# Optimization experiments

Measured on AMD Instinct MI355X. Metric: run time of the kernel, lower is better.

The kernel has to match this reference:

```python
import jax, jax.numpy as jnp
import numpy as np

B, N, M, C, H = 2, 256, 512, 256, 8
Dh = C // H          # head dim = 32
F = 256              # frequency_embedding_size
MAX_PERIOD = 10000.0


def setup_inputs() -> dict:
    rng = jax.random.key(0)
    ks = jax.random.split(rng, 12)
    s = 0.02

    def w(k, shape):
        return jax.random.normal(k, shape, jnp.float32) * s

    inp = {
        "query": jax.random.normal(ks[0], (B, N, C), jnp.float32),
        "key": jax.random.normal(ks[1], (B, M, C), jnp.float32),
        "query_pos": jax.random.uniform(ks[2], (B, N, M), jnp.float32),
        # attention projections (torch Linear stores W as (out,in))
        "Wq": w(ks[3], (C, C)), "bq": jnp.zeros((C,), jnp.float32),
        "Wk": w(ks[4], (C, C)),
        "Wv": w(ks[5], (C, C)), "bv": jnp.zeros((C,), jnp.float32),
        "Wo": w(ks[6], (C, C)), "bo": jnp.zeros((C,), jnp.float32),
        # ScalarEmbedder MLP: Linear(F, C) -> SiLU -> Linear(C, C)
        "W1": w(ks[7], (C, F)), "b1": jnp.zeros((C,), jnp.float32),
        "W2": w(ks[8], (C, C)), "b2": jnp.zeros((C,), jnp.float32),
        "freqs": jnp.exp(-np.log(MAX_PERIOD) * jnp.arange(F // 2, dtype=jnp.float32) / (F // 2)),
    }
    return inp


def reference(query, key, query_pos, Wq, bq, Wk, Wv, bv, Wo, bo, W1, b1, W2, b2, freqs):
    scale = Dh ** (-0.5)
    # projections -> (B, H, N/M, Dh)
    q = (query @ Wq.T + bq).reshape(B, N, H, Dh).transpose(0, 2, 1, 3)
    k = (key @ Wk.T).reshape(B, M, H, Dh).transpose(0, 2, 1, 3)
    v = (key @ Wv.T + bv).reshape(B, M, H, Dh).transpose(0, 2, 1, 3)
    # scalar positional embedding per (n, m) pair
    t = query_pos.reshape(-1)                              # (B*N*M,)
    tf = t[:, None] * freqs                                # (B*N*M, F/2)
    emb = jnp.concatenate([jnp.cos(tf), jnp.sin(tf)], -1)  # (B*N*M, F)
    pe = jax.nn.silu(emb @ W1.T + b1) @ W2.T + b2          # (B*N*M, C)
    pe = pe.reshape(B, N, M, H, Dh).transpose(0, 3, 1, 2, 4)  # (B,H,N,M,Dh)
    # gated scores: (q[:,:,:,None] * pe) . k  ==  einsum over d
    attn = jnp.einsum('bhnd,bhnmd,bhmd->bhnm', q, pe, k) * scale
    attn = jax.nn.softmax(attn, axis=-1)
    x = jnp.einsum('bhnm,bhmd->bhnd', attn, v)             # (B,H,N,Dh)
    x = x.transpose(0, 2, 1, 3).reshape(B, N, C)
    return x @ Wo.T + bo + query
```

## Files before the change

### kernel.cpp

```cpp
#include <hip/hip_runtime.h>

#define Bn 2
#define Nn 256
#define Mn 512
#define Cn 256
#define Hn 8
#define MT 128
#define SCALE_ 0.17677669529663687f
#define INV2PI 0.15915494309189535f

typedef short bf16x8 __attribute__((ext_vector_type(8)));
typedef short bf16x4 __attribute__((ext_vector_type(4)));
typedef float f32x4 __attribute__((ext_vector_type(4)));

static __device__ __forceinline__ float b2f(short s) {
    unsigned u = ((unsigned)(unsigned short)s) << 16;
    return __builtin_bit_cast(float, u);
}
static __device__ __forceinline__ short f2b(float f) {
    unsigned u = __builtin_bit_cast(unsigned, f);
    u += 0x7fffu + ((u >> 16) & 1u);
    return (short)(u >> 16);
}
static __device__ __forceinline__ void async16(const void* g, void* l) {
    __builtin_amdgcn_global_load_lds(
        (const __attribute__((address_space(1))) unsigned int*)g,
        (__attribute__((address_space(3))) unsigned int*)l, 16, 0, 0);
}

__global__ __launch_bounds__(256) void prep2(
        const float* __restrict__ key, const float* __restrict__ Wk,
        const float* __restrict__ Wv, const float* __restrict__ bv,
        const float* __restrict__ W1, const float* __restrict__ W2,
        short* __restrict__ W1b, short* __restrict__ W2b,
        short* __restrict__ kpb, short* __restrict__ vpb) {
    __shared__ float arow[32][Cn];
    const int bid = blockIdx.x;
    const int t = threadIdx.x;
    if (bid < 64) {
        const int half = bid >> 5;
        const int off = (bid & 31) * 2048 + t * 8;
        const float* src = half ? W2 : W1;
        short* dst = half ? W2b : W1b;
        const float4 a = *(const float4*)(src + off);
        const float4 c = *(const float4*)(src + off + 4);
        bf16x8 p;
        p[0] = f2b(a.x); p[1] = f2b(a.y); p[2] = f2b(a.z); p[3] = f2b(a.w);
        p[4] = f2b(c.x); p[5] = f2b(c.y); p[6] = f2b(c.z); p[7] = f2b(c.w);
        *(bf16x8*)(dst + off) = p;
        return;
    }
    const int isv = bid >= 320;
    const int id = bid - (isv ? 320 : 64);
    const int r0 = (id >> 3) * 32, c0 = (id & 7) * 32;
    const float* W = isv ? Wv : Wk;
    #pragma unroll
    for (int i = 0; i < 32; ++i) arow[i][t] = key[(size_t)(r0 + i) * Cn + t];
    __syncthreads();
    const int col = c0 + (t & 31);
    const int rs = t >> 5;
    float a4[4] = {0.f, 0.f, 0.f, 0.f};
    const float* wr = W + (size_t)col * Cn;
    for (int k = 0; k < Cn; k += 4) {
        const float4 wv = *(const float4*)(wr + k);
        #pragma unroll
        for (int i = 0; i < 4; ++i) {
            const int r = rs * 4 + i;
            a4[i] += arow[r][k] * wv.x + arow[r][k+1] * wv.y
                   + arow[r][k+2] * wv.z + arow[r][k+3] * wv.w;
        }
    }
    if (!isv) {
        const int bk = r0 >> 9, mm0 = (r0 & 511) + rs * 4;
        char* base = (char*)kpb + (size_t)bk * Mn * Cn * 2;
        #pragma unroll
        for (int i = 0; i < 4; ++i) {
            const int m = mm0 + i;
            *(short*)(base + m * 512 + ((col * 2) ^ ((m & 7) << 4))) = f2b(a4[i]);
        }
    } else {
        const float bvv = bv[col];
        #pragma unroll
        for (int i = 0; i < 4; ++i)
            vpb[(size_t)(r0 + rs * 4 + i) * Cn + col] = f2b(a4[i] + bvv);
    }
}

__global__ __launch_bounds__(512, 1) void fused_attn(
        const float* __restrict__ query, const float* __restrict__ Wq,
        const float* __restrict__ bq, const short* __restrict__ kpb,
        const short* __restrict__ vpb, const float* __restrict__ qpos,
        const short* __restrict__ W1b, const short* __restrict__ W2b,
        const float* __restrict__ b1, const float* __restrict__ b2,
        const float* __restrict__ freqs, const float* __restrict__ Wo,
        const float* __restrict__ bo, float* __restrict__ xout) {
    __shared__ __align__(16) char embS[MT * 512];
    __shared__ __align__(16) char kS[MT * 512];
    __shared__ float tposS[Mn];
    __shared__ float fbuf[128];
    __shared__ float qbuf[Cn];
    __shared__ float b2buf[Cn];
    __shared__ float scb2[Hn * MT];
    __shared__ float pacc[512];
    __shared__ float corrS[Hn], lS[Hn];

    const int t = threadIdx.x;
    const int lane = t & 63;
    const int w = t >> 6;
    const int lr = lane & 15, lg = lane >> 4;

    const int qrow = ((blockIdx.x & 7) << 6) | (blockIdx.x >> 3);
    const int b = qrow >> 8;

    const int cA = w * 32 + lr, cB = cA + 16;
    const short* w1p0 = W1b + (size_t)cA * Cn + lg * 8;
    const short* w1p1 = W1b + (size_t)cB * Cn + lg * 8;
    const short* w2p0 = W2b + (size_t)cA * Cn + lg * 8;
    const short* w2p1 = W2b + (size_t)cB * Cn + lg * 8;
    const float b1v0 = b1[cA], b1v1 = b1[cB];

    tposS[t] = qpos[(size_t)qrow * Mn + t];
    if (t < 128) fbuf[t] = freqs[t] * INV2PI;
    if (t < 256) {
        b2buf[t] = b2[t];
        scb2[t] = query[(size_t)qrow * Cn + t];
    }
    __syncthreads();
    {
        const int c = t & 255, half = t >> 8;
        const float* wr = Wq + (size_t)c * Cn + half * 128;
        const float* xb = scb2 + half * 128;
        float s = 0.f;
        for (int k = 0; k < 128; k += 4) {
            const float4 wv = *(const float4*)(wr + k);
            s += xb[k] * wv.x + xb[k+1] * wv.y + xb[k+2] * wv.z + xb[k+3] * wv.w;
        }
        pacc[t] = s;
    }
    __syncthreads();
    if (t < 256) qbuf[t] = (pacc[t] + pacc[t + 256] + bq[t]) * SCALE_;

    float m_run = -1e30f, l_run = 0.f;
    float xacc = 0.f;
    bf16x8 wreg[16];

    for (int m0 = 0; m0 < Mn; m0 += MT) {
        {
            const size_t tbase = ((size_t)(b * Mn + m0)) * Cn * 2;
            #pragma unroll
            for (int i = 0; i < 8; ++i) {
                const int seg = (i * 8 + w) * 1024;
                async16((const char*)kpb + tbase + seg + lane * 16, kS + seg);
            }
        }

        {
            const int m = t >> 2, fq = t & 3;
            const float tv = tposS[m0 + m];
            char* rowp = embS + m * 512;
            const int sw = (m & 7) << 4;
            #pragma unroll
            for (int j8 = 0; j8 < 4; ++j8) {
                bf16x8 pc, ps;
                #pragma unroll
                for (int e = 0; e < 8; ++e) {
                    const float xr = tv * fbuf[fq * 32 + j8 * 8 + e];
                    pc[e] = f2b(__builtin_amdgcn_cosf(xr));
                    ps[e] = f2b(__builtin_amdgcn_sinf(xr));
                }
                *(bf16x8*)(rowp + ((fq * 64 + j8 * 16) ^ sw)) = pc;
                *(bf16x8*)(rowp + ((256 + fq * 64 + j8 * 16) ^ sw)) = ps;
            }
        }
        __syncthreads();

        {
            int woff = 0;
            asm volatile("" : "+v"(woff));
            #pragma unroll
            for (int kk = 0; kk < 8; ++kk) {
                wreg[kk] = *(const bf16x8*)(w1p0 + woff + kk * 32);
                wreg[8 + kk] = *(const bf16x8*)(w1p1 + woff + kk * 32);
            }
        }
        f32x4 acc[8][2];
        #pragma unroll
        for (int pb = 0; pb < 8; ++pb) {
            acc[pb][0] = (f32x4){0.f, 0.f, 0.f, 0.f};
            acc[pb][1] = (f32x4){0.f, 0.f, 0.f, 0.f};
        }
        #pragma unroll
        for (int pb = 0; pb < 8; ++pb) {
            const int row = pb * 16 + lr;
            const int sw = (row & 7) << 4;
            const char* rowp = embS + row * 512;
            #pragma unroll
            for (int kk = 0; kk < 8; ++kk) {
                const bf16x8 a = *(const bf16x8*)(rowp + ((lg * 16 + kk * 64) ^ sw));
                acc[pb][0] = __builtin_amdgcn_mfma_f32_16x16x32_bf16(a, wreg[kk],     acc[pb][0], 0, 0, 0);
                acc[pb][1] = __builtin_amdgcn_mfma_f32_16x16x32_bf16(a, wreg[8 + kk], acc[pb][1], 0, 0, 0);
            }
        }
        __syncthreads();

        #pragma unroll
        for (int pb = 0; pb < 8; ++pb) {
            #pragma unroll
            for (int jb = 0; jb < 2; ++jb) {
                const float bv = jb ? b1v1 : b1v0;
                const int j = w * 32 + jb * 16 + lr;
                #pragma unroll
                for (int r = 0; r < 4; ++r) {
                    const int row = pb * 16 + lg * 4 + r;
                    float hv = acc[pb][jb][r] + bv;
                    hv = hv / (1.f + __expf(-hv));
                    *(short*)(embS + row * 512 + ((j * 2) ^ ((row & 7) << 4))) = f2b(hv);
                }
            }
        }
        __syncthreads();

        {
            int woff = 0;
            asm volatile("" : "+v"(woff));
            #pragma unroll
            for (int kk = 0; kk < 8; ++kk) {
                wreg[kk] = *(const bf16x8*)(w2p0 + woff + kk * 32);
                wreg[8 + kk] = *(const bf16x8*)(w2p1 + woff + kk * 32);
            }
        }
        {
            float b2a[8];
            #pragma unroll
            for (int i = 0; i < 8; ++i)
                b2a[i] = b2buf[w * 32 + (i >> 2) * 16 + lg * 4 + (i & 3)];
            #pragma unroll
            for (int mb = 0; mb < 8; ++mb)
                #pragma unroll
                for (int cb = 0; cb < 2; ++cb)
                    #pragma unroll
                    for (int r = 0; r < 4; ++r)
                        acc[mb][cb][r] = b2a[cb * 4 + r];
        }
        #pragma unroll
        for (int mb = 0; mb < 8; ++mb) {
            const int row = mb * 16 + lr;
            const int sw = (row & 7) << 4;
            const char* rowp = embS + row * 512;
            #pragma unroll
            for (int kk = 0; kk < 8; ++kk) {
                const bf16x8 a = *(const bf16x8*)(rowp + ((lg * 16 + kk * 64) ^ sw));
                acc[mb][0] = __builtin_amdgcn_mfma_f32_16x16x32_bf16(wreg[kk],     a, acc[mb][0], 0, 0, 0);
                acc[mb][1] = __builtin_amdgcn_mfma_f32_16x16x32_bf16(wreg[8 + kk], a, acc[mb][1], 0, 0, 0);
            }
        }

        {
            float qa[8];
            #pragma unroll
            for (int i = 0; i < 8; ++i)
                qa[i] = qbuf[w * 32 + (i >> 2) * 16 + lg * 4 + (i & 3)];
            #pragma unroll
            for (int mb = 0; mb < 8; ++mb) {
                const int m = mb * 16 + lr;
                const int sw = (m & 7) << 4;
                const char* kr = kS + m * 512;
                const int cc0 = (w * 32 + lg * 4) * 2;
                const bf16x4 k0 = *(const bf16x4*)(kr + (cc0 ^ sw));
                const bf16x4 k1 = *(const bf16x4*)(kr + ((cc0 + 32) ^ sw));
                float partial = 0.f;
                #pragma unroll
                for (int r = 0; r < 4; ++r) {
                    partial += qa[r] * b2f(k0[r]) * acc[mb][0][r]
                             + qa[4 + r] * b2f(k1[r]) * acc[mb][1][r];
                }
                partial += __shfl_xor(partial, 16);
                partial += __shfl_xor(partial, 32);
                if (lg == 0) scb2[w * MT + m] = partial;
            }
        }

        {
            const float s0 = scb2[w * MT + lane];
            const float s1 = scb2[w * MT + 64 + lane];
            float tmax = fmaxf(s0, s1);
            #pragma unroll
            for (int msk = 1; msk < 64; msk <<= 1) tmax = fmaxf(tmax, __shfl_xor(tmax, msk));
            const float mnew = fmaxf(m_run, tmax);
            const float corr = __expf(m_run - mnew);
            const float e0 = __expf(s0 - mnew);
            const float e1 = __expf(s1 - mnew);
            scb2[w * MT + lane] = e0;
            scb2[w * MT + 64 + lane] = e1;
            float ss = e0 + e1;
            #pragma unroll
            for (int msk = 1; msk < 64; msk <<= 1) ss += __shfl_xor(ss, msk);
            l_run = l_run * corr + ss;
            m_run = mnew;
            if (lane == 0) corrS[w] = corr;
        }
        __syncthreads();

        {
            const int c = t & 255, half = t >> 8;
            const int h = c >> 5;
            const short* vrow = vpb + ((size_t)(b * Mn + m0 + half * 64)) * Cn + c;
            const float* wr2 = scb2 + h * MT + half * 64;
            float s = 0.f;
            #pragma unroll
            for (int i = 0; i < 16; ++i) {
                const float4 wa = *(const float4*)(wr2 + i * 4);
                s += wa.x * b2f(vrow[(size_t)(i * 4 + 0) * Cn])
                   + wa.y * b2f(vrow[(size_t)(i * 4 + 1) * Cn])
                   + wa.z * b2f(vrow[(size_t)(i * 4 + 2) * Cn])
                   + wa.w * b2f(vrow[(size_t)(i * 4 + 3) * Cn]);
            }
            pacc[t] = s;
        }
        __syncthreads();
        if (t < 256) xacc = xacc * corrS[t >> 5] + pacc[t] + pacc[t + 256];
    }

    if (lane == 0) lS[w] = l_run;
    __syncthreads();
    if (t < 256) scb2[t] = xacc / lS[t >> 5];
    __syncthreads();
    {
        const int j = t & 255, half = t >> 8;
        const float* wr = Wo + (size_t)j * Cn + half * 128;
        const float* xb = scb2 + half * 128;
        float s = 0.f;
        for (int k = 0; k < 128; k += 4) {
            const float4 wv = *(const float4*)(wr + k);
            s += xb[k] * wv.x + xb[k+1] * wv.y + xb[k+2] * wv.z + xb[k+3] * wv.w;
        }
        pacc[t] = s;
    }
    __syncthreads();
    if (t < 256)
        xout[(size_t)qrow * Cn + t] = pacc[t] + pacc[t + 256] + bo[t]
                                    + query[(size_t)qrow * Cn + t];
}

extern "C" void kernel_launch(void* const* d_in, const int* in_sizes, int n_in,
                              void* d_out, int out_size, void* d_ws, size_t ws_size,
                              hipStream_t stream) {
    const float* query = (const float*)d_in[0];
    const float* key   = (const float*)d_in[1];
    const float* qpos  = (const float*)d_in[2];
    const float* Wq    = (const float*)d_in[3];
    const float* bq    = (const float*)d_in[4];
    const float* Wk    = (const float*)d_in[5];
    const float* Wv    = (const float*)d_in[6];
    const float* bv    = (const float*)d_in[7];
    const float* Wo    = (const float*)d_in[8];
    const float* bo    = (const float*)d_in[9];
    const float* W1    = (const float*)d_in[10];
    const float* b1    = (const float*)d_in[11];
    const float* W2    = (const float*)d_in[12];
    const float* b2    = (const float*)d_in[13];
    const float* freqs = (const float*)d_in[14];
    float* out = (float*)d_out;

    char* ws = (char*)d_ws;
    short* kpb = (short*)(ws);
    short* vpb = (short*)(ws + 524288);
    short* W1b = (short*)(ws + 1048576);
    short* W2b = (short*)(ws + 1179648);

    prep2<<<576, 256, 0, stream>>>(key, Wk, Wv, bv, W1, W2, W1b, W2b, kpb, vpb);
    fused_attn<<<Bn * Nn, 512, 0, stream>>>(query, Wq, bq, kpb, vpb, qpos,
                                            W1b, W2b, b1, b2, freqs, Wo, bo, out);
}
```

Baseline: 295.9 us.

## Halve M tile and double-buffer sinusoid embedding to overlap with MFMA work

Shrinks the key tile from 128 to 64 rows and double-buffers the sinusoidal embedding buffer. The next tile's cos/sin embedding is computed right after the first MLP GEMM, and the next K tile is prefetched after the softmax. Hoisting the W2 register loads and deferring the xacc accumulation to the start of the next iteration removes one barrier per tile. The aim is to hide the transcendental and async-load latency behind matrix work, at the cost of twice as many loop iterations and extra LDS for the second buffer.

```diff
diff --git a/kernel.cpp b/kernel.cpp
--- a/kernel.cpp
+++ b/kernel.cpp
@@ -5,7 +5,7 @@
 #define Mn 512
 #define Cn 256
 #define Hn 8
-#define MT 128
+#define MT 64
 #define SCALE_ 0.17677669529663687f
 #define INV2PI 0.15915494309189535f
 
@@ -94,7 +94,7 @@
         const float* __restrict__ b1, const float* __restrict__ b2,
         const float* __restrict__ freqs, const float* __restrict__ Wo,
         const float* __restrict__ bo, float* __restrict__ xout) {
-    __shared__ __align__(16) char embS[MT * 512];
+    __shared__ __align__(16) char embS[2][MT * 512];
     __shared__ __align__(16) char kS[MT * 512];
     __shared__ float tposS[Mn];
     __shared__ float fbuf[128];
@@ -119,6 +119,33 @@
     const short* w2p1 = W2b + (size_t)cB * Cn + lg * 8;
     const float b1v0 = b1[cA], b1v1 = b1[cB];
 
+    auto emb_compute = [&](int m0w, char* buf) {
+        const int m = t >> 3, fg = t & 7;
+        const float tv = tposS[(m0w + m) & (Mn - 1)];
+        char* rowp = buf + m * 512;
+        const int sw = (m & 7) << 4;
+        #pragma unroll
+        for (int j8 = 0; j8 < 2; ++j8) {
+            bf16x8 pc, ps;
+            #pragma unroll
+            for (int e = 0; e < 8; ++e) {
+                const float xr = tv * fbuf[fg * 16 + j8 * 8 + e];
+                pc[e] = f2b(__builtin_amdgcn_cosf(xr));
+                ps[e] = f2b(__builtin_amdgcn_sinf(xr));
+            }
+            *(bf16x8*)(rowp + ((fg * 32 + j8 * 16) ^ sw)) = pc;
+            *(bf16x8*)(rowp + ((256 + fg * 32 + j8 * 16) ^ sw)) = ps;
+        }
+    };
+    auto stage_k = [&](int m0w) {
+        const size_t tbase = ((size_t)(b * Mn + (m0w & (Mn - 1)))) * Cn * 2;
+        #pragma unroll
+        for (int i = 0; i < 4; ++i) {
+            const int seg = (i * 8 + w) * 1024;
+            async16((const char*)kpb + tbase + seg + lane * 16, kS + seg);
+        }
+    };
+
     tposS[t] = qpos[(size_t)qrow * Mn + t];
     if (t < 128) fbuf[t] = freqs[t] * INV2PI;
     if (t < 256) {
@@ -139,40 +166,20 @@
     }
     __syncthreads();
     if (t < 256) qbuf[t] = (pacc[t] + pacc[t + 256] + bq[t]) * SCALE_;
+    emb_compute(0, embS[0]);
+    stage_k(0);
 
     float m_run = -1e30f, l_run = 0.f;
     float xacc = 0.f;
     bf16x8 wreg[16];
 
-    for (int m0 = 0; m0 < Mn; m0 += MT) {
-        {
-            const size_t tbase = ((size_t)(b * Mn + m0)) * Cn * 2;
-            #pragma unroll
-            for (int i = 0; i < 8; ++i) {
-                const int seg = (i * 8 + w) * 1024;
-                async16((const char*)kpb + tbase + seg + lane * 16, kS + seg);
-            }
-        }
-
-        {
-            const int m = t >> 2, fq = t & 3;
-            const float tv = tposS[m0 + m];
-            char* rowp = embS + m * 512;
-            const int sw = (m & 7) << 4;
-            #pragma unroll
-            for (int j8 = 0; j8 < 4; ++j8) {
-                bf16x8 pc, ps;
-                #pragma unroll
-                for (int e = 0; e < 8; ++e) {
-                    const float xr = tv * fbuf[fq * 32 + j8 * 8 + e];
-                    pc[e] = f2b(__builtin_amdgcn_cosf(xr));
-                    ps[e] = f2b(__builtin_amdgcn_sinf(xr));
-                }
-                *(bf16x8*)(rowp + ((fq * 64 + j8 * 16) ^ sw)) = pc;
-                *(bf16x8*)(rowp + ((256 + fq * 64 + j8 * 16) ^ sw)) = ps;
-            }
-        }
+    for (int tix = 0; tix < Mn / MT; ++tix) {
+        const int m0 = tix * MT;
+        char* bufc = embS[tix & 1];
+        char* bufn = embS[(tix + 1) & 1];
+
         __syncthreads();
+        if (tix > 0 && t < 256) xacc = xacc * corrS[t >> 5] + pacc[t] + pacc[t + 256];
 
         {
             int woff = 0;
@@ -183,17 +190,17 @@
                 wreg[8 + kk] = *(const bf16x8*)(w1p1 + woff + kk * 32);
             }
         }
-        f32x4 acc[8][2];
-        #pragma unroll
-        for (int pb = 0; pb < 8; ++pb) {
+        f32x4 acc[4][2];
+        #pragma unroll
+        for (int pb = 0; pb < 4; ++pb) {
             acc[pb][0] = (f32x4){0.f, 0.f, 0.f, 0.f};
             acc[pb][1] = (f32x4){0.f, 0.f, 0.f, 0.f};
         }
         #pragma unroll
-        for (int pb = 0; pb < 8; ++pb) {
+        for (int pb = 0; pb < 4; ++pb) {
             const int row = pb * 16 + lr;
             const int sw = (row & 7) << 4;
-            const char* rowp = embS + row * 512;
+            const char* rowp = bufc + row * 512;
             #pragma unroll
             for (int kk = 0; kk < 8; ++kk) {
                 const bf16x8 a = *(const bf16x8*)(rowp + ((lg * 16 + kk * 64) ^ sw));
@@ -201,10 +208,20 @@
                 acc[pb][1] = __builtin_amdgcn_mfma_f32_16x16x32_bf16(a, wreg[8 + kk], acc[pb][1], 0, 0, 0);
             }
         }
+        emb_compute(m0 + MT, bufn);
         __syncthreads();
 
-        #pragma unroll
-        for (int pb = 0; pb < 8; ++pb) {
+        {
+            int woff = 0;
+            asm volatile("" : "+v"(woff));
+            #pragma unroll
+            for (int kk = 0; kk < 8; ++kk) {
+                wreg[kk] = *(const bf16x8*)(w2p0 + woff + kk * 32);
+                wreg[8 + kk] = *(const bf16x8*)(w2p1 + woff + kk * 32);
+            }
+        }
+        #pragma unroll
+        for (int pb = 0; pb < 4; ++pb) {
             #pragma unroll
             for (int jb = 0; jb < 2; ++jb) {
                 const float bv = jb ? b1v1 : b1v0;
@@ -214,28 +231,19 @@
                     const int row = pb * 16 + lg * 4 + r;
                     float hv = acc[pb][jb][r] + bv;
                     hv = hv / (1.f + __expf(-hv));
-                    *(short*)(embS + row * 512 + ((j * 2) ^ ((row & 7) << 4))) = f2b(hv);
+                    *(short*)(bufc + row * 512 + ((j * 2) ^ ((row & 7) << 4))) = f2b(hv);
                 }
             }
         }
         __syncthreads();
 
-        {
-            int woff = 0;
-            asm volatile("" : "+v"(woff));
-            #pragma unroll
-            for (int kk = 0; kk < 8; ++kk) {
-                wreg[kk] = *(const bf16x8*)(w2p0 + woff + kk * 32);
-                wreg[8 + kk] = *(const bf16x8*)(w2p1 + woff + kk * 32);
-            }
-        }
         {
             float b2a[8];
             #pragma unroll
             for (int i = 0; i < 8; ++i)
                 b2a[i] = b2buf[w * 32 + (i >> 2) * 16 + lg * 4 + (i & 3)];
             #pragma unroll
-            for (int mb = 0; mb < 8; ++mb)
+            for (int mb = 0; mb < 4; ++mb)
                 #pragma unroll
                 for (int cb = 0; cb < 2; ++cb)
                     #pragma unroll
@@ -243,10 +251,10 @@
                         acc[mb][cb][r] = b2a[cb * 4 + r];
         }
         #pragma unroll
-        for (int mb = 0; mb < 8; ++mb) {
+        for (int mb = 0; mb < 4; ++mb) {
             const int row = mb * 16 + lr;
             const int sw = (row & 7) << 4;
-            const char* rowp = embS + row * 512;
+            const char* rowp = bufc + row * 512;
             #pragma unroll
             for (int kk = 0; kk < 8; ++kk) {
                 const bf16x8 a = *(const bf16x8*)(rowp + ((lg * 16 + kk * 64) ^ sw));
@@ -261,7 +269,7 @@
             for (int i = 0; i < 8; ++i)
                 qa[i] = qbuf[w * 32 + (i >> 2) * 16 + lg * 4 + (i & 3)];
             #pragma unroll
-            for (int mb = 0; mb < 8; ++mb) {
+            for (int mb = 0; mb < 4; ++mb) {
                 const int m = mb * 16 + lr;
                 const int sw = (m & 7) << 4;
                 const char* kr = kS + m * 512;
@@ -281,18 +289,15 @@
         }
 
         {
-            const float s0 = scb2[w * MT + lane];
-            const float s1 = scb2[w * MT + 64 + lane];
-            float tmax = fmaxf(s0, s1);
+            const float s = scb2[w * MT + lane];
+            float tmax = s;
             #pragma unroll
             for (int msk = 1; msk < 64; msk <<= 1) tmax = fmaxf(tmax, __shfl_xor(tmax, msk));
             const float mnew = fmaxf(m_run, tmax);
             const float corr = __expf(m_run - mnew);
-            const float e0 = __expf(s0 - mnew);
-            const float e1 = __expf(s1 - mnew);
-            scb2[w * MT + lane] = e0;
-            scb2[w * MT + 64 + lane] = e1;
-            float ss = e0 + e1;
+            const float e = __expf(s - mnew);
+            scb2[w * MT + lane] = e;
+            float ss = e;
             #pragma unroll
             for (int msk = 1; msk < 64; msk <<= 1) ss += __shfl_xor(ss, msk);
             l_run = l_run * corr + ss;
@@ -301,14 +306,16 @@
         }
         __syncthreads();
 
+        stage_k(m0 + MT);
+
         {
             const int c = t & 255, half = t >> 8;
             const int h = c >> 5;
-            const short* vrow = vpb + ((size_t)(b * Mn + m0 + half * 64)) * Cn + c;
-            const float* wr2 = scb2 + h * MT + half * 64;
+            const short* vrow = vpb + ((size_t)(b * Mn + m0 + half * 32)) * Cn + c;
+            const float* wr2 = scb2 + h * MT + half * 32;
             float s = 0.f;
             #pragma unroll
-            for (int i = 0; i < 16; ++i) {
+            for (int i = 0; i < 8; ++i) {
                 const float4 wa = *(const float4*)(wr2 + i * 4);
                 s += wa.x * b2f(vrow[(size_t)(i * 4 + 0) * Cn])
                    + wa.y * b2f(vrow[(size_t)(i * 4 + 1) * Cn])
@@ -317,9 +324,9 @@
             }
             pacc[t] = s;
         }
-        __syncthreads();
-        if (t < 256) xacc = xacc * corrS[t >> 5] + pacc[t] + pacc[t + 256];
-    }
+    }
+    __syncthreads();
+    if (t < 256) xacc = xacc * corrS[t >> 5] + pacc[t] + pacc[t + 256];
 
     if (lane == 0) lS[w] = l_run;
     __syncthreads();
```

Result: slower. 333.7 us (+12.8%).
